# Optimization experiments

Hardware: AMD Instinct MI355X
Metric: run time of the kernel (lower is better)

The kernel has to match this reference:

```python
import jax, jax.numpy as jnp
import numpy as np

N = 4096          # N_TARGET_NODES (node count == feature dim)
E = 262144        # number of directed edges (avg degree 64)


def setup_inputs() -> dict:
    key = jax.random.key(0)
    k1, k2, k3, k4 = jax.random.split(key, 4)
    x = jax.random.normal(k1, (N, N), dtype=jnp.float32)
    edge_index = jax.random.randint(k2, (2, E), 0, N, dtype=jnp.int32)
    # scale weights so sigmoid inputs are O(1)
    W1 = jax.random.normal(k3, (N, N), dtype=jnp.float32) * (1.0 / np.sqrt(N))
    b1 = jnp.zeros((N,), dtype=jnp.float32)
    W2 = jax.random.normal(k4, (N, 1), dtype=jnp.float32) * (1.0 / np.sqrt(N))
    b2 = jnp.zeros((1,), dtype=jnp.float32)
    return {"x": x, "edge_index": edge_index, "W1": W1, "b1": b1, "W2": W2, "b2": b2}


def _gcn_conv(x, edge_index, W, b):
    """PyG GCNConv: h = D^{-1/2}(A+I)D^{-1/2} (x W) + b, edge weights = 1."""
    n = x.shape[0]
    h = x @ W                                   # [n, out]
    loop = jnp.arange(n, dtype=edge_index.dtype)
    src = jnp.concatenate([edge_index[0], loop])  # add self loops
    dst = jnp.concatenate([edge_index[1], loop])
    deg = jax.ops.segment_sum(jnp.ones_like(src, dtype=h.dtype), dst, num_segments=n)
    dinv = jnp.where(deg > 0, jax.lax.rsqrt(deg), 0.0)
    norm = dinv[src] * dinv[dst]                # [E+n]
    msg = h[src] * norm[:, None]                # gather + scale
    out = jax.ops.segment_sum(msg, dst, num_segments=n)  # scatter-add at targets
    return out + b


def reference(x, edge_index, W1, b1, W2, b2):
    # torch.squeeze(x) is a no-op for 2-D x
    x1 = jax.nn.sigmoid(_gcn_conv(x, edge_index, W1, b1))
    # F.dropout in eval mode is identity (deterministic reference)
    x2 = jax.nn.sigmoid(_gcn_conv(x1, edge_index, W2, b2))
    return x2  # [N, 1]
```

## Files before the change

### kernel.cpp

```cpp
#include <hip/hip_runtime.h>


typedef __attribute__((ext_vector_type(8))) short bf16x8;
typedef __attribute__((ext_vector_type(4))) float f32x4;

#define NN 4096
#define NT 64

__device__ __forceinline__ unsigned f2bf(float f) {
  unsigned u = __float_as_uint(f);
  return (u + 0x7FFFu + ((u >> 16) & 1u)) >> 16;
}

#define GLDS(g, l) __builtin_amdgcn_global_load_lds(                      \
    (const __attribute__((address_space(1))) void*)(g),                   \
    (__attribute__((address_space(3))) void*)(l), 16, 0, 0)


__global__ void init_deg_kernel(float* deg) {
  int v = blockIdx.x * 256 + threadIdx.x;
  if (v < NN) deg[v] = 1.0f;
}

__global__ void count_deg_kernel(const int* __restrict__ dst, int E, float* deg) {
  int e = blockIdx.x * 256 + threadIdx.x;
  if (e < E) atomicAdd(&deg[dst[e]], 1.0f);
}

__global__ void dinv_kernel(const float* __restrict__ deg, float* __restrict__ dinv) {
  int v = blockIdx.x * 256 + threadIdx.x;
  if (v < NN) dinv[v] = rsqrtf(deg[v]);
}

__global__ void diag_kernel(const float* __restrict__ dinv, float* __restrict__ S) {
  int v = blockIdx.x * 256 + threadIdx.x;
  if (v < NN) { float d = dinv[v]; S[(size_t)v * NN + v] = d * d; }
}

__global__ void scatter_S_kernel(const int* __restrict__ src, const int* __restrict__ dst,
                                 int E, const float* __restrict__ dinv, float* __restrict__ S) {
  int e = blockIdx.x * 256 + threadIdx.x;
  if (e < E) {
    int s = src[e], d = dst[e];
    atomicAdd(&S[(size_t)d * NN + s], dinv[s] * dinv[d]);
  }
}


__global__ void cast_kernel(const float* __restrict__ in, unsigned short* __restrict__ out, int n) {
  int i = (blockIdx.x * 256 + threadIdx.x) * 8;
  if (i >= n) return;
  const float4* p = (const float4*)(in + i);
  float4 a = p[0], b = p[1];
  uint4 o;
  o.x = f2bf(a.x) | (f2bf(a.y) << 16);
  o.y = f2bf(a.z) | (f2bf(a.w) << 16);
  o.z = f2bf(b.x) | (f2bf(b.y) << 16);
  o.w = f2bf(b.z) | (f2bf(b.w) << 16);
  *(uint4*)(out + i) = o;
}

__global__ void transpose_cast_kernel(const float* __restrict__ W, unsigned short* __restrict__ WT) {
  __shared__ float tile[32][33];
  int bx = blockIdx.x * 32, by = blockIdx.y * 32;
  int tx = threadIdx.x, ty = threadIdx.y;
#pragma unroll
  for (int i = 0; i < 32; i += 8)
    tile[ty + i][tx] = W[(size_t)(by + ty + i) * NN + bx + tx];
  __syncthreads();
#pragma unroll
  for (int i = 0; i < 32; i += 8)
    WT[(size_t)(bx + ty + i) * NN + by + tx] = (unsigned short)f2bf(tile[tx][ty + i]);
}


template <int EPI>
__global__ __launch_bounds__(512, 2) void gemm256_kernel(
    const unsigned short* __restrict__ A, const unsigned short* __restrict__ BT,
    unsigned short* __restrict__ C, const float* __restrict__ bias) {
  __shared__ __align__(16) char smem[131072];
  const int tid = threadIdx.x;
  const int lane = tid & 63, wid = tid >> 6;
  const int wr = wid >> 2, wc = wid & 3;

  const int bid = blockIdx.x;
  const int swz = (bid & 7) * 32 + (bid >> 3);
  const int rowBase = (swz >> 4) * 256;
  const int colBase = (swz & 15) * 256;

  const int srow = tid >> 3;
  const int scolb = ((tid & 7) << 4) ^ ((srow & 7) << 4);
  const unsigned short* pA = A + (size_t)(rowBase + srow) * NN + (scolb >> 1);
  const unsigned short* pB = BT + (size_t)(colBase + srow) * NN + (scolb >> 1);

  const int rl = lane & 15;
  const int c0 = ((lane >> 4) << 4) ^ ((lane & 7) << 4);
  const int c1 = c0 ^ 64;
  const int aoff = (wr * 128 + rl) * 128;
  const int boff = 32768 + (wc * 64 + rl) * 128;

  f32x4 acc[8][4] = {};
  bf16x8 bk0[4], bk1[4], afA[4], afB[4];

  {
    char* w0 = smem + (wid << 10);
    GLDS(pB + (size_t)0 * 64 * NN, w0 + 32768 + 0 * 8192);
    GLDS(pB + (size_t)1 * 64 * NN, w0 + 32768 + 1 * 8192);
    GLDS(pB + (size_t)2 * 64 * NN, w0 + 32768 + 2 * 8192);
    GLDS(pB + (size_t)3 * 64 * NN, w0 + 32768 + 3 * 8192);
    GLDS(pA + (size_t)0 * 64 * NN, w0 + 0 * 8192);
    GLDS(pA + (size_t)2 * 64 * NN, w0 + 2 * 8192);
    GLDS(pA + (size_t)1 * 64 * NN, w0 + 1 * 8192);
    GLDS(pA + (size_t)3 * 64 * NN, w0 + 3 * 8192);
    asm volatile("s_waitcnt vmcnt(2)" ::: "memory");
    __builtin_amdgcn_s_barrier();
#pragma unroll
    for (int m = 0; m < 4; ++m) afA[m] = *(const bf16x8*)(smem + aoff + m * 2048 + c0);
#pragma unroll
    for (int n = 0; n < 4; ++n) bk0[n] = *(const bf16x8*)(smem + boff + n * 2048 + c0);
  }

#pragma unroll 2
  for (int t = 0; t < NT; ++t) {
    const char* lb = smem + ((t & 1) << 16);
    char* st = smem + (((t & 1) ^ 1) << 16) + (wid << 10);
    const unsigned short* s1A = pA + ((t + 1) & 63) * 64;
    const unsigned short* s1B = pB + ((t + 1) & 63) * 64;

    GLDS(s1B + (size_t)0 * 64 * NN, st + 32768 + 0 * 8192);
    GLDS(s1B + (size_t)1 * 64 * NN, st + 32768 + 1 * 8192);
    GLDS(s1B + (size_t)2 * 64 * NN, st + 32768 + 2 * 8192);
#pragma unroll
    for (int m = 0; m < 4; ++m) afB[m] = *(const bf16x8*)(lb + aoff + m * 2048 + c1);
#pragma unroll
    for (int n = 0; n < 4; ++n) bk1[n] = *(const bf16x8*)(lb + boff + n * 2048 + c1);
    __builtin_amdgcn_s_setprio(1);
#pragma unroll
    for (int m = 0; m < 4; ++m)
#pragma unroll
      for (int n = 0; n < 4; ++n)
        acc[m][n] = __builtin_amdgcn_mfma_f32_16x16x32_bf16(afA[m], bk0[n], acc[m][n], 0, 0, 0);
    __builtin_amdgcn_s_setprio(0);
    asm volatile("s_waitcnt vmcnt(3)" ::: "memory");
    __builtin_amdgcn_sched_barrier(0);

    GLDS(s1B + (size_t)3 * 64 * NN, st + 32768 + 3 * 8192);
    GLDS(s1A + (size_t)0 * 64 * NN, st + 0 * 8192);
    GLDS(s1A + (size_t)2 * 64 * NN, st + 2 * 8192);
#pragma unroll
    for (int m = 0; m < 4; ++m) afA[m] = *(const bf16x8*)(lb + aoff + (4 + m) * 2048 + c0);
    __builtin_amdgcn_s_setprio(1);
#pragma unroll
    for (int m = 0; m < 4; ++m)
#pragma unroll
      for (int n = 0; n < 4; ++n)
        acc[m][n] = __builtin_amdgcn_mfma_f32_16x16x32_bf16(afB[m], bk1[n], acc[m][n], 0, 0, 0);
    __builtin_amdgcn_s_setprio(0);
    __builtin_amdgcn_sched_barrier(0);

    GLDS(s1A + (size_t)1 * 64 * NN, st + 1 * 8192);
    GLDS(s1A + (size_t)3 * 64 * NN, st + 3 * 8192);
#pragma unroll
    for (int m = 0; m < 4; ++m) afB[m] = *(const bf16x8*)(lb + aoff + (4 + m) * 2048 + c1);
    __builtin_amdgcn_s_setprio(1);
#pragma unroll
    for (int m = 0; m < 4; ++m)
#pragma unroll
      for (int n = 0; n < 4; ++n)
        acc[4 + m][n] = __builtin_amdgcn_mfma_f32_16x16x32_bf16(afA[m], bk0[n], acc[4 + m][n], 0, 0, 0);
    __builtin_amdgcn_s_setprio(0);
    __builtin_amdgcn_sched_barrier(0);

    __builtin_amdgcn_s_setprio(1);
#pragma unroll
    for (int m = 0; m < 4; ++m)
#pragma unroll
      for (int n = 0; n < 4; ++n)
        acc[4 + m][n] = __builtin_amdgcn_mfma_f32_16x16x32_bf16(afB[m], bk1[n], acc[4 + m][n], 0, 0, 0);
    __builtin_amdgcn_s_setprio(0);
    asm volatile("s_waitcnt lgkmcnt(0)" ::: "memory");
    asm volatile("s_waitcnt vmcnt(2)" ::: "memory");
    __builtin_amdgcn_s_barrier();
    {
      const char* nb = smem + (((t + 1) & 1) << 16);
#pragma unroll
      for (int m = 0; m < 4; ++m) afA[m] = *(const bf16x8*)(nb + aoff + m * 2048 + c0);
#pragma unroll
      for (int n = 0; n < 4; ++n) bk0[n] = *(const bf16x8*)(nb + boff + n * 2048 + c0);
    }
    __builtin_amdgcn_sched_barrier(0);
  }

  const int orow = rowBase + wr * 128 + (lane >> 4) * 4;
  const int ocol = colBase + wc * 64 + (lane & 15);
#pragma unroll
  for (int n = 0; n < 4; ++n) {
    int ccol = ocol + n * 16;
    float bv = (EPI == 1) ? bias[ccol] : 0.0f;
#pragma unroll
    for (int m = 0; m < 8; ++m) {
#pragma unroll
      for (int i = 0; i < 4; ++i) {
        float x = acc[m][n][i] + bv;
        if (EPI == 1) x = 1.0f / (1.0f + __expf(-x));
        C[(size_t)(orow + m * 16 + i) * NN + ccol] = (unsigned short)f2bf(x);
      }
    }
  }
}


__global__ void matvec_kernel(const unsigned short* __restrict__ X1,
                              const float* __restrict__ W2, float* __restrict__ h2) {
  int row = blockIdx.x, t = threadIdx.x;
  const unsigned short* xr = X1 + (size_t)row * NN;
  float s = 0.0f;
  for (int j = t * 8; j < NN; j += 2048) {
    uint4 u = *(const uint4*)(xr + j);
    unsigned v[4] = {u.x, u.y, u.z, u.w};
#pragma unroll
    for (int q = 0; q < 4; ++q) {
      float lo = __uint_as_float(v[q] << 16);
      float hi = __uint_as_float(v[q] & 0xFFFF0000u);
      s += lo * W2[j + q * 2] + hi * W2[j + q * 2 + 1];
    }
  }
#pragma unroll
  for (int off = 32; off > 0; off >>= 1) s += __shfl_down(s, off);
  __shared__ float wsum[4];
  if ((t & 63) == 0) wsum[t >> 6] = s;
  __syncthreads();
  if (t == 0) h2[row] = wsum[0] + wsum[1] + wsum[2] + wsum[3];
}

__global__ void init_t_kernel(const float* __restrict__ dinv, const float* __restrict__ h2,
                              const float* __restrict__ b2, float* __restrict__ tacc) {
  int v = blockIdx.x * 256 + threadIdx.x;
  if (v < NN) tacc[v] = dinv[v] * dinv[v] * h2[v] + b2[0];
}

__global__ void scatter_t_kernel(const int* __restrict__ src, const int* __restrict__ dst,
                                 int E, const float* __restrict__ dinv,
                                 const float* __restrict__ h2, float* __restrict__ tacc) {
  int e = blockIdx.x * 256 + threadIdx.x;
  if (e < E) {
    int s = src[e], d = dst[e];
    atomicAdd(&tacc[d], dinv[s] * dinv[d] * h2[s]);
  }
}

__global__ void final_kernel(const float* __restrict__ tacc, float* __restrict__ out) {
  int v = blockIdx.x * 256 + threadIdx.x;
  if (v < NN) out[v] = 1.0f / (1.0f + __expf(-tacc[v]));
}


extern "C" void kernel_launch(void* const* d_in, const int* in_sizes, int n_in,
                              void* d_out, int out_size, void* d_ws, size_t ws_size,
                              hipStream_t stream) {
  const float* x  = (const float*)d_in[0];
  const int*   ei = (const int*)d_in[1];
  const float* W1 = (const float*)d_in[2];
  const float* b1 = (const float*)d_in[3];
  const float* W2 = (const float*)d_in[4];
  const float* b2 = (const float*)d_in[5];
  float* out = (float*)d_out;
  const int E = in_sizes[1] / 2;
  const int* esrc = ei;
  const int* edst = ei + E;

  char* w = (char*)d_ws;
  float*          Sf  = (float*)w;
  unsigned short* H1T = (unsigned short*)w;
  unsigned short* W1T = (unsigned short*)(w + (size_t)(32u << 20));
  unsigned short* Sbf = (unsigned short*)(w + (size_t)(64u << 20));
  unsigned short* Xbf = (unsigned short*)(w + (size_t)(96u << 20));
  float* deg  = (float*)(w + (size_t)(128u << 20));
  float* dinv = deg + 4096;
  float* h2   = deg + 8192;
  float* tacc = deg + 12288;

  init_deg_kernel<<<16, 256, 0, stream>>>(deg);
  count_deg_kernel<<<(E + 255) / 256, 256, 0, stream>>>(edst, E, deg);
  dinv_kernel<<<16, 256, 0, stream>>>(deg, dinv);

  hipMemsetAsync(Sf, 0, (size_t)64 << 20, stream);
  diag_kernel<<<16, 256, 0, stream>>>(dinv, Sf);
  scatter_S_kernel<<<(E + 255) / 256, 256, 0, stream>>>(esrc, edst, E, dinv, Sf);
  cast_kernel<<<8192, 256, 0, stream>>>(Sf, Sbf, NN * NN);

  cast_kernel<<<8192, 256, 0, stream>>>(x, Xbf, NN * NN);
  transpose_cast_kernel<<<dim3(128, 128), dim3(32, 8), 0, stream>>>(W1, W1T);

  gemm256_kernel<0><<<256, 512, 0, stream>>>(W1T, Xbf, H1T, nullptr);
  gemm256_kernel<1><<<256, 512, 0, stream>>>(Sbf, H1T, Xbf, b1);

  matvec_kernel<<<4096, 256, 0, stream>>>(Xbf, W2, h2);
  init_t_kernel<<<16, 256, 0, stream>>>(dinv, h2, b2, tacc);
  scatter_t_kernel<<<(E + 255) / 256, 256, 0, stream>>>(esrc, edst, E, dinv, h2, tacc);
  final_kernel<<<16, 256, 0, stream>>>(tacc, out);
}
```

Baseline: 353.6 us.

## Fuse W2 matvec into second GEMM epilogue and move barrier earlier

The sigmoid output of the second GEMM is no longer written to memory. Instead it is multiplied by W2 inside the epilogue, reduced across lanes with shuffles, and atomically added into h2, so the separate matvec kernel and the 32MB bf16 write/read are removed. h2 is now zeroed with a memset first. The main loop also moves the barrier and the next-tile LDS fragment loads ahead of the last MFMA group so the loads overlap that compute. The cost is 16x more atomics into h2 and a nondeterministic summation order.

```diff
diff --git a/kernel.cpp b/kernel.cpp
--- a/kernel.cpp
+++ b/kernel.cpp
@@ -77,7 +77,8 @@
 template <int EPI>
 __global__ __launch_bounds__(512, 2) void gemm256_kernel(
     const unsigned short* __restrict__ A, const unsigned short* __restrict__ BT,
-    unsigned short* __restrict__ C, const float* __restrict__ bias) {
+    unsigned short* __restrict__ C, const float* __restrict__ bias,
+    const float* __restrict__ W2, float* __restrict__ h2) {
   __shared__ __align__(16) char smem[131072];
   const int tid = threadIdx.x;
   const int lane = tid & 63, wid = tid >> 6;
@@ -169,8 +170,18 @@
       for (int n = 0; n < 4; ++n)
         acc[4 + m][n] = __builtin_amdgcn_mfma_f32_16x16x32_bf16(afA[m], bk0[n], acc[4 + m][n], 0, 0, 0);
     __builtin_amdgcn_s_setprio(0);
+    asm volatile("s_waitcnt lgkmcnt(0)" ::: "memory");
+    asm volatile("s_waitcnt vmcnt(2)" ::: "memory");
+    __builtin_amdgcn_s_barrier();
     __builtin_amdgcn_sched_barrier(0);
 
+    {
+      const char* nb = smem + (((t + 1) & 1) << 16);
+#pragma unroll
+      for (int m = 0; m < 4; ++m) afA[m] = *(const bf16x8*)(nb + aoff + m * 2048 + c0);
+#pragma unroll
+      for (int n = 0; n < 4; ++n) bk0[n] = *(const bf16x8*)(nb + boff + n * 2048 + c0);
+    }
     __builtin_amdgcn_s_setprio(1);
 #pragma unroll
     for (int m = 0; m < 4; ++m)
@@ -178,60 +189,47 @@
       for (int n = 0; n < 4; ++n)
         acc[4 + m][n] = __builtin_amdgcn_mfma_f32_16x16x32_bf16(afB[m], bk1[n], acc[4 + m][n], 0, 0, 0);
     __builtin_amdgcn_s_setprio(0);
-    asm volatile("s_waitcnt lgkmcnt(0)" ::: "memory");
-    asm volatile("s_waitcnt vmcnt(2)" ::: "memory");
-    __builtin_amdgcn_s_barrier();
-    {
-      const char* nb = smem + (((t + 1) & 1) << 16);
-#pragma unroll
-      for (int m = 0; m < 4; ++m) afA[m] = *(const bf16x8*)(nb + aoff + m * 2048 + c0);
-#pragma unroll
-      for (int n = 0; n < 4; ++n) bk0[n] = *(const bf16x8*)(nb + boff + n * 2048 + c0);
-    }
     __builtin_amdgcn_sched_barrier(0);
   }
 
   const int orow = rowBase + wr * 128 + (lane >> 4) * 4;
   const int ocol = colBase + wc * 64 + (lane & 15);
-#pragma unroll
-  for (int n = 0; n < 4; ++n) {
-    int ccol = ocol + n * 16;
-    float bv = (EPI == 1) ? bias[ccol] : 0.0f;
-#pragma unroll
-    for (int m = 0; m < 8; ++m) {
-#pragma unroll
-      for (int i = 0; i < 4; ++i) {
-        float x = acc[m][n][i] + bv;
-        if (EPI == 1) x = 1.0f / (1.0f + __expf(-x));
-        C[(size_t)(orow + m * 16 + i) * NN + ccol] = (unsigned short)f2bf(x);
+  if (EPI == 0) {
+#pragma unroll
+    for (int n = 0; n < 4; ++n) {
+      int ccol = ocol + n * 16;
+#pragma unroll
+      for (int m = 0; m < 8; ++m) {
+#pragma unroll
+        for (int i = 0; i < 4; ++i) {
+          C[(size_t)(orow + m * 16 + i) * NN + ccol] = (unsigned short)f2bf(acc[m][n][i]);
+        }
       }
     }
-  }
-}
-
-
-__global__ void matvec_kernel(const unsigned short* __restrict__ X1,
-                              const float* __restrict__ W2, float* __restrict__ h2) {
-  int row = blockIdx.x, t = threadIdx.x;
-  const unsigned short* xr = X1 + (size_t)row * NN;
-  float s = 0.0f;
-  for (int j = t * 8; j < NN; j += 2048) {
-    uint4 u = *(const uint4*)(xr + j);
-    unsigned v[4] = {u.x, u.y, u.z, u.w};
-#pragma unroll
-    for (int q = 0; q < 4; ++q) {
-      float lo = __uint_as_float(v[q] << 16);
-      float hi = __uint_as_float(v[q] & 0xFFFF0000u);
-      s += lo * W2[j + q * 2] + hi * W2[j + q * 2 + 1];
+  } else {
+    float bv[4], wv[4];
+#pragma unroll
+    for (int n = 0; n < 4; ++n) { bv[n] = bias[ocol + n * 16]; wv[n] = W2[ocol + n * 16]; }
+#pragma unroll
+    for (int m = 0; m < 8; ++m) {
+#pragma unroll
+      for (int i = 0; i < 4; ++i) {
+        float s = 0.0f;
+#pragma unroll
+        for (int n = 0; n < 4; ++n) {
+          float x = 1.0f / (1.0f + __expf(-(acc[m][n][i] + bv[n])));
+          s += x * wv[n];
+        }
+        s += __shfl_xor(s, 1);
+        s += __shfl_xor(s, 2);
+        s += __shfl_xor(s, 4);
+        s += __shfl_xor(s, 8);
+        if ((lane & 15) == 0) atomicAdd(&h2[orow + m * 16 + i], s);
+      }
     }
   }
-#pragma unroll
-  for (int off = 32; off > 0; off >>= 1) s += __shfl_down(s, off);
-  __shared__ float wsum[4];
-  if ((t & 63) == 0) wsum[t >> 6] = s;
-  __syncthreads();
-  if (t == 0) h2[row] = wsum[0] + wsum[1] + wsum[2] + wsum[3];
-}
+}
+
 
 __global__ void init_t_kernel(const float* __restrict__ dinv, const float* __restrict__ h2,
                               const float* __restrict__ b2, float* __restrict__ tacc) {
@@ -285,6 +283,7 @@
   dinv_kernel<<<16, 256, 0, stream>>>(deg, dinv);
 
   hipMemsetAsync(Sf, 0, (size_t)64 << 20, stream);
+  hipMemsetAsync(h2, 0, 4096 * sizeof(float), stream);
   diag_kernel<<<16, 256, 0, stream>>>(dinv, Sf);
   scatter_S_kernel<<<(E + 255) / 256, 256, 0, stream>>>(esrc, edst, E, dinv, Sf);
   cast_kernel<<<8192, 256, 0, stream>>>(Sf, Sbf, NN * NN);
@@ -292,10 +291,9 @@
   cast_kernel<<<8192, 256, 0, stream>>>(x, Xbf, NN * NN);
   transpose_cast_kernel<<<dim3(128, 128), dim3(32, 8), 0, stream>>>(W1, W1T);
 
-  gemm256_kernel<0><<<256, 512, 0, stream>>>(W1T, Xbf, H1T, nullptr);
-  gemm256_kernel<1><<<256, 512, 0, stream>>>(Sbf, H1T, Xbf, b1);
-
-  matvec_kernel<<<4096, 256, 0, stream>>>(Xbf, W2, h2);
+  gemm256_kernel<0><<<256, 512, 0, stream>>>(W1T, Xbf, H1T, nullptr, nullptr, nullptr);
+  gemm256_kernel<1><<<256, 512, 0, stream>>>(Sbf, H1T, nullptr, b1, W2, h2);
+
   init_t_kernel<<<16, 256, 0, stream>>>(dinv, h2, b2, tacc);
   scatter_t_kernel<<<(E + 255) / 256, 256, 0, stream>>>(esrc, edst, E, dinv, h2, tacc);
   final_kernel<<<16, 256, 0, stream>>>(tacc, out);
```

Result: faster. 345.3 us (-2.4%).
